# Performance work log

Hardware: AMD Instinct MI355X
Metric: run time of the kernel (lower is better)

## Reference

```python
import jax, jax.numpy as jnp
import numpy as np

B, T, D, H = 4, 2048, 1024, 16
HS = D // H  # head_size = 64
EPS = 1e-5


def _layernorm(x, g, b):
    mu = jnp.mean(x, axis=-1, keepdims=True)
    var = jnp.var(x, axis=-1, keepdims=True)
    return (x - mu) * jax.lax.rsqrt(var + EPS) * g + b


def setup_inputs() -> dict:
    key = jax.random.key(0)
    ks = jax.random.split(key, 12)
    s = lambda fan_in: 1.0 / np.sqrt(fan_in)
    return {
        "x": jax.random.normal(ks[0], (B, T, D), dtype=jnp.float32),
        # per-head projections, stacked: (H, D, HS)
        "Wq": jax.random.uniform(ks[1], (H, D, HS), jnp.float32, -s(D), s(D)),
        "Wk": jax.random.uniform(ks[2], (H, D, HS), jnp.float32, -s(D), s(D)),
        "Wv": jax.random.uniform(ks[3], (H, D, HS), jnp.float32, -s(D), s(D)),
        "Wo": jax.random.uniform(ks[4], (D, D), jnp.float32, -s(D), s(D)),
        "bo": jax.random.uniform(ks[5], (D,), jnp.float32, -s(D), s(D)),
        "W1": jax.random.uniform(ks[6], (D, 4 * D), jnp.float32, -s(D), s(D)),
        "b1": jax.random.uniform(ks[7], (4 * D,), jnp.float32, -s(D), s(D)),
        "W2": jax.random.uniform(ks[8], (4 * D, D), jnp.float32, -s(4 * D), s(4 * D)),
        "b2": jax.random.uniform(ks[9], (D,), jnp.float32, -s(4 * D), s(4 * D)),
        "g1": jnp.ones((D,), jnp.float32),
        "be1": jnp.zeros((D,), jnp.float32),
        "g2": jnp.ones((D,), jnp.float32),
        "be2": jnp.zeros((D,), jnp.float32),
    }


def reference(x, Wq, Wk, Wv, Wo, bo, W1, b1, W2, b2, g1, be1, g2, be2):
    # --- self-attention sublayer (pre-LN) ---
    h = _layernorm(x, g1, be1)                       # (B,T,D)
    q = jnp.einsum('btd,hds->bhts', h, Wq)           # (B,H,T,HS)
    k = jnp.einsum('btd,hds->bhts', h, Wk)
    v = jnp.einsum('btd,hds->bhts', h, Wv)
    scores = jnp.einsum('bhts,bhus->bhtu', q, k) * (HS ** -0.5)  # (B,H,T,T)
    causal = jnp.tril(jnp.ones((T, T), dtype=bool))
    scores = jnp.where(causal, scores, -jnp.inf)
    w = jax.nn.softmax(scores, axis=-1)
    attn = jnp.einsum('bhtu,bhus->bhts', w, v)       # (B,H,T,HS)
    attn = attn.transpose(0, 2, 1, 3).reshape(B, T, D)  # concat heads
    x = x + attn @ Wo + bo
    # --- feed-forward sublayer (pre-LN) ---
    h2 = _layernorm(x, g2, be2)
    x = x + jax.nn.relu(h2 @ W1 + b1) @ W2 + b2
    return x
```

## Files before the change

kernel.cpp:

```cpp
#include <hip/hip_runtime.h>
#include <hip/hip_bf16.h>
#include <cstddef>

#define B_ 4
#define T_ 2048
#define D_ 1024
#define H_ 16
#define HS_ 64
#define QS_ 3072

typedef short short8 __attribute__((ext_vector_type(8)));
typedef float f32x4 __attribute__((ext_vector_type(4)));

__device__ __forceinline__ unsigned short f2b(float x) {
    __hip_bfloat16 b = __float2bfloat16(x);
    return *reinterpret_cast<unsigned short*>(&b);
}

__device__ __forceinline__ void gload_lds16(const void* g, void* l) {
    __builtin_amdgcn_global_load_lds((const __attribute__((address_space(1))) void*)g,
                                     (__attribute__((address_space(3))) void*)l, 16, 0, 0);
}

__global__ __launch_bounds__(256) void ln_kernel(const float* __restrict__ X,
                                                 const float* __restrict__ g,
                                                 const float* __restrict__ be,
                                                 unsigned short* __restrict__ O)
{
    const int row = blockIdx.x;
    const int tid = threadIdx.x;
    const float* xr = X + (size_t)row * D_;
    float4 xv = *reinterpret_cast<const float4*>(xr + tid * 4);
    float s  = xv.x + xv.y + xv.z + xv.w;
    float s2 = xv.x * xv.x + xv.y * xv.y + xv.z * xv.z + xv.w * xv.w;
#pragma unroll
    for (int off = 32; off > 0; off >>= 1) {
        s  += __shfl_xor(s,  off);
        s2 += __shfl_xor(s2, off);
    }
    __shared__ float red[8];
    const int wid = tid >> 6, lane = tid & 63;
    if (lane == 0) { red[wid * 2] = s; red[wid * 2 + 1] = s2; }
    __syncthreads();
    s  = red[0] + red[2] + red[4] + red[6];
    s2 = red[1] + red[3] + red[5] + red[7];
    const float mu  = s * (1.0f / D_);
    const float var = s2 * (1.0f / D_) - mu * mu;
    const float r   = rsqrtf(var + 1e-5f);
    float4 gv = *reinterpret_cast<const float4*>(g  + tid * 4);
    float4 bv = *reinterpret_cast<const float4*>(be + tid * 4);
    ushort4 ov;
    ov.x = f2b((xv.x - mu) * r * gv.x + bv.x);
    ov.y = f2b((xv.y - mu) * r * gv.y + bv.y);
    ov.z = f2b((xv.z - mu) * r * gv.z + bv.z);
    ov.w = f2b((xv.w - mu) * r * gv.w + bv.w);
    *reinterpret_cast<ushort4*>(O + (size_t)row * D_ + tid * 4) = ov;
}

__global__ __launch_bounds__(256) void transpose_all(const float* __restrict__ Wq,
                                                     const float* __restrict__ Wk,
                                                     const float* __restrict__ Wv,
                                                     const float* __restrict__ Wo,
                                                     const float* __restrict__ W1,
                                                     const float* __restrict__ W2,
                                                     unsigned short* __restrict__ Wtqkv,
                                                     unsigned short* __restrict__ Wto,
                                                     unsigned short* __restrict__ Wt1,
                                                     unsigned short* __restrict__ Wt2)
{
    __shared__ float tile[32][33];
    const int tx = threadIdx.x & 31, ty = threadIdx.x >> 5;
    int s = blockIdx.x;

    if (s < 3072) {
        const float* in = (s < 1024) ? Wq : (s < 2048) ? Wk : Wv;
        const int noff = (s < 1024) ? 0 : (s < 2048) ? D_ : 2 * D_;
        s &= 1023;
        const int bn = (s & 31) * 32, bk = (s >> 5) * 32;
        const int head = bn >> 6, s0 = bn & 63;
#pragma unroll
        for (int i = 0; i < 32; i += 8)
            tile[ty + i][tx] = in[(size_t)head * D_ * HS_ + (size_t)(bk + ty + i) * HS_ + s0 + tx];
        __syncthreads();
#pragma unroll
        for (int i = 0; i < 32; i += 8)
            Wtqkv[(size_t)(noff + bn + ty + i) * D_ + bk + tx] = f2b(tile[tx][ty + i]);
        return;
    }
    s -= 3072;
    const float* in; unsigned short* out; int K, N, bn, bk;
    if (s < 1024)      { in = Wo; out = Wto; K = D_;     N = D_;     bn = (s & 31) * 32;  bk = (s >> 5) * 32; }
    else if (s < 5120) { s -= 1024; in = W1; out = Wt1; K = D_;     N = 4 * D_; bn = (s & 127) * 32; bk = (s >> 7) * 32; }
    else               { s -= 5120; in = W2; out = Wt2; K = 4 * D_; N = D_;     bn = (s & 31) * 32;  bk = (s >> 5) * 32; }
#pragma unroll
    for (int i = 0; i < 32; i += 8)
        tile[ty + i][tx] = in[(size_t)(bk + ty + i) * N + bn + tx];
    __syncthreads();
#pragma unroll
    for (int i = 0; i < 32; i += 8)
        out[(size_t)(bn + ty + i) * K + bk + tx] = f2b(tile[tx][ty + i]);
}

template<bool BIAS, bool RELU, bool RESID, bool OUT_BF16, bool SCALEQ>
__global__ __launch_bounds__(512, 1) void gemm_sq(const unsigned short* __restrict__ A,
                                                  const unsigned short* __restrict__ Bt,
                                                  const float* __restrict__ bias,
                                                  const float* __restrict__ resid,
                                                  float* __restrict__ Cf,
                                                  unsigned short* __restrict__ Cb,
                                                  int M, int N, int K)
{
    constexpr int BUFS = 16384 + 16384;
    __shared__ __attribute__((aligned(128))) unsigned short lds[2 * BUFS];

    const int tid = threadIdx.x, l = tid & 63, w = tid >> 6;
    const int wRow = w >> 2, wCol = w & 3;
    const int lr = l & 15, lq = l >> 4;

    const int gx = gridDim.x;
    const int nwg = gx * (int)gridDim.y;
    const int orig = (int)blockIdx.y * gx + (int)blockIdx.x;
    const int xcd = orig & 7, lo = orig >> 3;
    const int q8 = nwg >> 3, r8 = nwg & 7;
    const int wg = (xcd < r8 ? xcd * (q8 + 1) : r8 * (q8 + 1) + (xcd - r8) * q8) + lo;
    const int bm = wg / gx, bn = wg % gx;

    const int nt = K >> 6;

    auto ISSUE_HALF = [&](int t, int half) {
        const size_t kof = (size_t)t * 64;
        const int buf = t & 1;
        const unsigned short* src = (half < 2) ? A : Bt;
        const int rb = ((half < 2) ? bm : bn) * 256 + (half & 1) * 128;
        const int lb = buf * BUFS + ((half >= 2) ? 16384 : 0) + (half & 1) * 128 * 64;
#pragma unroll
        for (int p = 0; p < 2; ++p) {
            const int j = p * 512 + tid;
            const int row = j >> 3, ci = j & 7;
            gload_lds16(src + (size_t)(rb + row) * K + kof + ((ci ^ (row & 7)) * 8),
                        &lds[lb + j * 8]);
        }
    };

    f32x4 acc[8][4];
#pragma unroll
    for (int i = 0; i < 8; ++i)
#pragma unroll
        for (int j = 0; j < 4; ++j) acc[i][j] = (f32x4){0.f, 0.f, 0.f, 0.f};

    short8 af[4][2], bf[4][2];
    const int swz = lr & 7;

#pragma unroll
    for (int h = 0; h < 4; ++h) ISSUE_HALF(0, h);

    for (int t = 0; t < nt; ++t) {
        const unsigned short* As = &lds[(t & 1) * BUFS];
        const unsigned short* Bs = As + 16384;
        const bool more = (t + 1 < nt);

        asm volatile("s_waitcnt vmcnt(0)" ::: "memory");
        __builtin_amdgcn_s_barrier();

        if (more) ISSUE_HALF(t + 1, 0);
#pragma unroll
        for (int mi = 0; mi < 4; ++mi) {
            const int row = wRow * 128 + mi * 16 + lr;
#pragma unroll
            for (int ks = 0; ks < 2; ++ks)
                af[mi][ks] = *reinterpret_cast<const short8*>(&As[row * 64 + (((ks * 4 + lq) ^ swz) * 8)]);
        }
#pragma unroll
        for (int nj = 0; nj < 2; ++nj) {
            const int rowB = wCol * 64 + nj * 16 + lr;
#pragma unroll
            for (int ks = 0; ks < 2; ++ks)
                bf[nj][ks] = *reinterpret_cast<const short8*>(&Bs[rowB * 64 + (((ks * 4 + lq) ^ swz) * 8)]);
        }
        asm volatile("s_waitcnt lgkmcnt(0)" ::: "memory");
        __builtin_amdgcn_sched_barrier(0);
        __builtin_amdgcn_s_setprio(1);
#pragma unroll
        for (int mi = 0; mi < 4; ++mi)
#pragma unroll
            for (int nj = 0; nj < 2; ++nj)
#pragma unroll
                for (int ks = 0; ks < 2; ++ks)
                    acc[mi][nj] = __builtin_amdgcn_mfma_f32_16x16x32_bf16(af[mi][ks], bf[nj][ks], acc[mi][nj], 0, 0, 0);
        __builtin_amdgcn_s_setprio(0);

        if (more) ISSUE_HALF(t + 1, 1);
#pragma unroll
        for (int nj = 2; nj < 4; ++nj) {
            const int rowB = wCol * 64 + nj * 16 + lr;
#pragma unroll
            for (int ks = 0; ks < 2; ++ks)
                bf[nj][ks] = *reinterpret_cast<const short8*>(&Bs[rowB * 64 + (((ks * 4 + lq) ^ swz) * 8)]);
        }
        asm volatile("s_waitcnt lgkmcnt(0)" ::: "memory");
        __builtin_amdgcn_sched_barrier(0);
        __builtin_amdgcn_s_setprio(1);
#pragma unroll
        for (int mi = 0; mi < 4; ++mi)
#pragma unroll
            for (int nj = 2; nj < 4; ++nj)
#pragma unroll
                for (int ks = 0; ks < 2; ++ks)
                    acc[mi][nj] = __builtin_amdgcn_mfma_f32_16x16x32_bf16(af[mi][ks], bf[nj][ks], acc[mi][nj], 0, 0, 0);
        __builtin_amdgcn_s_setprio(0);

        if (more) { ISSUE_HALF(t + 1, 2); ISSUE_HALF(t + 1, 3); }
#pragma unroll
        for (int mi = 0; mi < 4; ++mi) {
            const int row = wRow * 128 + (4 + mi) * 16 + lr;
#pragma unroll
            for (int ks = 0; ks < 2; ++ks)
                af[mi][ks] = *reinterpret_cast<const short8*>(&As[row * 64 + (((ks * 4 + lq) ^ swz) * 8)]);
        }
        asm volatile("s_waitcnt lgkmcnt(0)" ::: "memory");
        __builtin_amdgcn_sched_barrier(0);
        __builtin_amdgcn_s_setprio(1);
#pragma unroll
        for (int mi = 0; mi < 4; ++mi)
#pragma unroll
            for (int nj = 0; nj < 2; ++nj)
#pragma unroll
                for (int ks = 0; ks < 2; ++ks)
                    acc[4 + mi][nj] = __builtin_amdgcn_mfma_f32_16x16x32_bf16(af[mi][ks], bf[nj][ks], acc[4 + mi][nj], 0, 0, 0);
        __builtin_amdgcn_s_setprio(0);

        __builtin_amdgcn_s_setprio(1);
#pragma unroll
        for (int mi = 0; mi < 4; ++mi)
#pragma unroll
            for (int nj = 2; nj < 4; ++nj)
#pragma unroll
                for (int ks = 0; ks < 2; ++ks)
                    acc[4 + mi][nj] = __builtin_amdgcn_mfma_f32_16x16x32_bf16(af[mi][ks], bf[nj][ks], acc[4 + mi][nj], 0, 0, 0);
        __builtin_amdgcn_s_setprio(0);
    }

    const int m0 = bm * 256 + wRow * 128;
    const int n0 = bn * 256 + wCol * 64;
#pragma unroll
    for (int nf = 0; nf < 4; ++nf) {
        const int col = n0 + nf * 16 + lr;
        const float bv = BIAS ? bias[col] : 0.0f;
#pragma unroll
        for (int mf = 0; mf < 8; ++mf) {
#pragma unroll
            for (int r = 0; r < 4; ++r) {
                const int row = m0 + mf * 16 + lq * 4 + r;
                float c = acc[mf][nf][r] + bv;
                if (RELU) c = fmaxf(c, 0.0f);
                if (RESID) c += resid[(size_t)row * N + col];
                if (SCALEQ) { if (col < D_) c *= 0.18033688f; }
                if (OUT_BF16) Cb[(size_t)row * N + col] = f2b(c);
                else          Cf[(size_t)row * N + col] = c;
            }
        }
    }
}

template<bool BIAS, bool RELU, bool RESID, bool OUT_BF16, bool SCALEQ, bool VSPLIT>
__global__ __launch_bounds__(512, 1) void gemm_sq2(const unsigned short* __restrict__ A,
                                                   const unsigned short* __restrict__ Bt,
                                                   const float* __restrict__ bias,
                                                   const float* __restrict__ resid,
                                                   float* __restrict__ Cf,
                                                   unsigned short* __restrict__ Cb,
                                                   unsigned short* __restrict__ Vt,
                                                   int M, int N, int K)
{
    constexpr int BUFS = 8192 + 16384;
    __shared__ __attribute__((aligned(128))) unsigned short lds[3 * BUFS];

    const int tid = threadIdx.x, l = tid & 63, w = tid >> 6;
    const int wRow = w >> 2, wCol = w & 3;
    const int lr = l & 15, lq = l >> 4;

    const int gx = gridDim.x;
    const int nwg = gx * (int)gridDim.y;
    const int orig = (int)blockIdx.y * gx + (int)blockIdx.x;
    const int xcd = orig & 7, lo = orig >> 3;
    const int q8 = nwg >> 3, r8 = nwg & 7;
    const int wg = (xcd < r8 ? xcd * (q8 + 1) : r8 * (q8 + 1) + (xcd - r8) * q8) + lo;
    const int bm = wg / gx, bn = wg % gx;

    const int nt = K >> 6;

    auto ISSUE = [&](int t, int buf) {
        const size_t kof = (size_t)t * 64;
#pragma unroll
        for (int p = 0; p < 2; ++p) {
            const int j = p * 512 + tid;
            const int row = j >> 3, ci = j & 7;
            gload_lds16(A + (size_t)(bm * 128 + row) * K + kof + ((ci ^ (row & 7)) * 8),
                        &lds[buf * BUFS + j * 8]);
        }
#pragma unroll
        for (int p = 0; p < 4; ++p) {
            const int j = p * 512 + tid;
            const int row = j >> 3, ci = j & 7;
            gload_lds16(Bt + (size_t)(bn * 256 + row) * K + kof + ((ci ^ (row & 7)) * 8),
                        &lds[buf * BUFS + 8192 + j * 8]);
        }
    };

    f32x4 acc[4][4];
#pragma unroll
    for (int i = 0; i < 4; ++i)
#pragma unroll
        for (int j = 0; j < 4; ++j) acc[i][j] = (f32x4){0.f, 0.f, 0.f, 0.f};

    short8 af[2][2], bf[4][2];
    const int swz = lr & 7;

    ISSUE(0, 0);
    ISSUE(1, 1);

    for (int t = 0; t < nt; ++t) {
        const unsigned short* As = &lds[(t % 3) * BUFS];
        const unsigned short* Bs = As + 8192;
        if (t + 1 < nt) asm volatile("s_waitcnt vmcnt(6)" ::: "memory");
        else            asm volatile("s_waitcnt vmcnt(0)" ::: "memory");
        __builtin_amdgcn_s_barrier();
        if (t + 2 < nt) ISSUE(t + 2, (t + 2) % 3);

#pragma unroll
        for (int mi = 0; mi < 2; ++mi) {
            const int row = wRow * 64 + mi * 16 + lr;
#pragma unroll
            for (int ks = 0; ks < 2; ++ks)
                af[mi][ks] = *reinterpret_cast<const short8*>(&As[row * 64 + (((ks * 4 + lq) ^ swz) * 8)]);
        }
#pragma unroll
        for (int nj = 0; nj < 4; ++nj) {
            const int rowB = wCol * 64 + nj * 16 + lr;
#pragma unroll
            for (int ks = 0; ks < 2; ++ks)
                bf[nj][ks] = *reinterpret_cast<const short8*>(&Bs[rowB * 64 + (((ks * 4 + lq) ^ swz) * 8)]);
        }
        asm volatile("s_waitcnt lgkmcnt(0)" ::: "memory");
        __builtin_amdgcn_sched_barrier(0);
        __builtin_amdgcn_s_setprio(1);
#pragma unroll
        for (int mi = 0; mi < 2; ++mi)
#pragma unroll
            for (int nj = 0; nj < 4; ++nj)
#pragma unroll
                for (int ks = 0; ks < 2; ++ks)
                    acc[mi][nj] = __builtin_amdgcn_mfma_f32_16x16x32_bf16(af[mi][ks], bf[nj][ks], acc[mi][nj], 0, 0, 0);
        __builtin_amdgcn_s_setprio(0);

#pragma unroll
        for (int mi = 0; mi < 2; ++mi) {
            const int row = wRow * 64 + (2 + mi) * 16 + lr;
#pragma unroll
            for (int ks = 0; ks < 2; ++ks)
                af[mi][ks] = *reinterpret_cast<const short8*>(&As[row * 64 + (((ks * 4 + lq) ^ swz) * 8)]);
        }
        asm volatile("s_waitcnt lgkmcnt(0)" ::: "memory");
        __builtin_amdgcn_sched_barrier(0);
        __builtin_amdgcn_s_setprio(1);
#pragma unroll
        for (int mi = 0; mi < 2; ++mi)
#pragma unroll
            for (int nj = 0; nj < 4; ++nj)
#pragma unroll
                for (int ks = 0; ks < 2; ++ks)
                    acc[2 + mi][nj] = __builtin_amdgcn_mfma_f32_16x16x32_bf16(af[mi][ks], bf[nj][ks], acc[2 + mi][nj], 0, 0, 0);
        __builtin_amdgcn_s_setprio(0);
    }

    if (VSPLIT && bn >= 8) {
        __syncthreads();
        unsigned short* ldsT = lds;
        const int n0l = wCol * 64;
        const int m0l = wRow * 64;
#pragma unroll
        for (int nf = 0; nf < 4; ++nf) {
            const int cl = n0l + nf * 16 + lr;
#pragma unroll
            for (int mf = 0; mf < 4; ++mf) {
#pragma unroll
                for (int r = 0; r < 4; ++r) {
                    const int rl = m0l + mf * 16 + lq * 4 + r;
                    const int pos = (rl & 64) + (((rl & 15) << 2) | ((rl >> 4) & 3));
                    ldsT[cl * 136 + pos] = f2b(acc[mf][nf][r]);
                }
            }
        }
        __syncthreads();
        const int rowT = tid >> 1, half = tid & 1;
        const int colV = bn * 256 + rowT - 2 * D_;
        const int hd = colV >> 6, sdim = colV & 63;
        const int bb = bm >> 4;
        const int tt0 = (bm & 15) * 128 + half * 64;
        unsigned short* dst = Vt + (((size_t)(bb * H_ + hd) * 64 + sdim) << 11) + tt0;
        const unsigned short* srcl = &ldsT[rowT * 136 + half * 64];
#pragma unroll
        for (int i = 0; i < 8; ++i)
            *reinterpret_cast<short8*>(dst + i * 8) =
                *reinterpret_cast<const short8*>(srcl + i * 8);
        return;
    }

    const int m0 = bm * 128 + wRow * 64;
    const int n0 = bn * 256 + wCol * 64;
#pragma unroll
    for (int nf = 0; nf < 4; ++nf) {
        const int col = n0 + nf * 16 + lr;
        const float bv = BIAS ? bias[col] : 0.0f;
#pragma unroll
        for (int mf = 0; mf < 4; ++mf) {
#pragma unroll
            for (int r = 0; r < 4; ++r) {
                const int row = m0 + mf * 16 + lq * 4 + r;
                float c = acc[mf][nf][r] + bv;
                if (RELU) c = fmaxf(c, 0.0f);
                if (RESID) c += resid[(size_t)row * N + col];
                if (SCALEQ) { if (col < D_) c *= 0.18033688f; }
                if (OUT_BF16) Cb[(size_t)row * N + col] = f2b(c);
                else          Cf[(size_t)row * N + col] = c;
            }
        }
    }
}

template<bool MASKED>
__device__ __forceinline__ void attn_chunk(
    const unsigned short* __restrict__ ksb,
    const unsigned short* __restrict__ vsb,
    unsigned short (* __restrict__ psw)[72],
    const short8* aq, f32x4* o,
    int lr, int lq, int wl)
{
    const short8 vone = {0x3F80, 0x3F80, 0x3F80, 0x3F80, 0x3F80, 0x3F80, 0x3F80, 0x3F80};
    f32x4 s[4];
#pragma unroll
    for (int kb = 0; kb < 4; ++kb) s[kb] = (f32x4){0.f, 0.f, 0.f, 0.f};
    __builtin_amdgcn_s_setprio(1);
#pragma unroll
    for (int kb = 0; kb < 4; ++kb) {
        if (MASKED && kb > wl) continue;
        const int row = kb * 16 + lr;
        const int sw = row & 7;
#pragma unroll
        for (int ks = 0; ks < 2; ++ks) {
            const int ch = (ks * 4 + lq) ^ sw;
            const short8 bk = *reinterpret_cast<const short8*>(&ksb[row * 64 + ch * 8]);
            s[kb] = __builtin_amdgcn_mfma_f32_16x16x32_bf16(aq[ks], bk, s[kb], 0, 0, 0);
        }
    }
    __builtin_amdgcn_s_setprio(0);

#pragma unroll
    for (int r = 0; r < 4; ++r) {
        const int qloc = wl * 16 + lq * 4 + r;
        float p[4];
#pragma unroll
        for (int kb = 0; kb < 4; ++kb) {
            const bool msk = MASKED && (kb * 16 + lr > qloc);
            p[kb] = msk ? 0.0f : exp2f(s[kb][r]);
        }
        const unsigned int w0 = (unsigned int)f2b(p[0]) | ((unsigned int)f2b(p[1]) << 16);
        const unsigned int w1 = (unsigned int)f2b(p[2]) | ((unsigned int)f2b(p[3]) << 16);
        uint2 pk; pk.x = w0; pk.y = w1;
        *reinterpret_cast<uint2*>(&psw[lq * 4 + r][lr * 4]) = pk;
    }
    asm volatile("s_waitcnt lgkmcnt(0)" ::: "memory");
    __builtin_amdgcn_s_setprio(1);
#pragma unroll
    for (int ks = 0; ks < 2; ++ks) {
        const short8 pa = *reinterpret_cast<const short8*>(&psw[lr][ks * 32 + lq * 8]);
#pragma unroll
        for (int df = 0; df < 4; ++df) {
            const int vrow = df * 16 + lr;
            const int vch = (ks * 4 + lq) ^ (vrow & 7);
            const short8 vb = *reinterpret_cast<const short8*>(&vsb[vrow * 64 + vch * 8]);
            o[df] = __builtin_amdgcn_mfma_f32_16x16x32_bf16(pa, vb, o[df], 0, 0, 0);
        }
        o[4] = __builtin_amdgcn_mfma_f32_16x16x32_bf16(pa, vone, o[4], 0, 0, 0);
    }
    __builtin_amdgcn_s_setprio(0);
}

__global__ __launch_bounds__(512, 4) void attn_mfma(const unsigned short* __restrict__ QKV,
                                                    const unsigned short* __restrict__ Vt,
                                                    unsigned short* __restrict__ Og)
{
    __shared__ __attribute__((aligned(128))) unsigned short Ks[2][64 * 64];
    __shared__ __attribute__((aligned(128))) unsigned short Vs[2][64 * 64];
    __shared__ __attribute__((aligned(16)))  unsigned short Ps[8][16][72];

    const int NQT = T_ / 128;
    const int px = blockIdx.x;
    const int qtA = px, qtB = NQT - 1 - px;
    const int h = blockIdx.y, b = blockIdx.z;
    const int tid = threadIdx.x, w = tid >> 6, l = tid & 63;
    const int wl = w & 3, qsub = w >> 2;
    const int lr = l & 15, lq = l >> 4;
    const size_t base = (size_t)b * T_ * QS_ + h * HS_;

    short8 aqA[2], aqB[2];
    {
        const int qrl = qsub * 64 + wl * 16 + lr;
        const unsigned short* pA = QKV + base + (size_t)(qtA * 128 + qrl) * QS_;
        const unsigned short* pB = QKV + base + (size_t)(qtB * 128 + qrl) * QS_;
        aqA[0] = *reinterpret_cast<const short8*>(pA + lq * 8);
        aqA[1] = *reinterpret_cast<const short8*>(pA + 32 + lq * 8);
        aqB[0] = *reinterpret_cast<const short8*>(pB + lq * 8);
        aqB[1] = *reinterpret_cast<const short8*>(pB + 32 + lq * 8);
    }

    const unsigned short* Kg = QKV + D_;
    const unsigned short* Vg = Vt + ((size_t)(b * H_ + h) * 64 << 11);

    auto stage = [&](int c, int bf) {
        const int kbase = c * 64;
        const int row = tid >> 3;
        const int cx = ((tid & 7) ^ (row & 7)) * 8;
        gload_lds16(Kg + base + (size_t)(kbase + row) * QS_ + cx, &Ks[bf][tid * 8]);
        gload_lds16(Vg + ((size_t)row << 11) + kbase + cx, &Vs[bf][tid * 8]);
    };

    stage(0, 0);
    __syncthreads();

    unsigned short (*psw)[72] = Ps[w];

    f32x4 oA[5], oB[5];
#pragma unroll
    for (int df = 0; df < 5; ++df) {
        oA[df] = (f32x4){0.f, 0.f, 0.f, 0.f};
        oB[df] = (f32x4){0.f, 0.f, 0.f, 0.f};
    }

    const int qminw = qsub * 64 + wl * 16;
    const int qmaxw = qminw + 15;

    const int nch = 2 * qtB + 2;
    int bf = 0;
    for (int c = 0; c < nch; ++c) {
        if (c + 1 < nch) stage(c + 1, bf ^ 1);
        const int relA = c * 64 - qtA * 128;
        const int relB = c * 64 - qtB * 128;
        if (relA <= qmaxw) {
            if (relA + 63 <= qminw)
                attn_chunk<false>(&Ks[bf][0], &Vs[bf][0], psw, aqA, oA, lr, lq, wl);
            else
                attn_chunk<true>(&Ks[bf][0], &Vs[bf][0], psw, aqA, oA, lr, lq, wl);
        }
        if (relB <= qmaxw) {
            if (relB + 63 <= qminw)
                attn_chunk<false>(&Ks[bf][0], &Vs[bf][0], psw, aqB, oB, lr, lq, wl);
            else
                attn_chunk<true>(&Ks[bf][0], &Vs[bf][0], psw, aqB, oB, lr, lq, wl);
        }
        if (c + 1 < nch) __syncthreads();
        bf ^= 1;
    }

    const size_t obase = (size_t)b * T_ * D_ + h * HS_;
#pragma unroll
    for (int r = 0; r < 4; ++r) {
        const float invA = 1.0f / oA[4][r];
        const float invB = 1.0f / oB[4][r];
        const int qrl = qsub * 64 + wl * 16 + lq * 4 + r;
        unsigned short* orowA = Og + obase + (size_t)(qtA * 128 + qrl) * D_;
        unsigned short* orowB = Og + obase + (size_t)(qtB * 128 + qrl) * D_;
#pragma unroll
        for (int df = 0; df < 4; ++df) {
            orowA[df * 16 + lr] = f2b(oA[df][r] * invA);
            orowB[df * 16 + lr] = f2b(oB[df][r] * invB);
        }
    }
}

extern "C" void kernel_launch(void* const* d_in, const int* in_sizes, int n_in,
                              void* d_out, int out_size, void* d_ws, size_t ws_size,
                              hipStream_t stream)
{
    const float* x   = (const float*)d_in[0];
    const float* Wq  = (const float*)d_in[1];
    const float* Wk  = (const float*)d_in[2];
    const float* Wv  = (const float*)d_in[3];
    const float* Wo  = (const float*)d_in[4];
    const float* bo  = (const float*)d_in[5];
    const float* W1  = (const float*)d_in[6];
    const float* b1  = (const float*)d_in[7];
    const float* W2  = (const float*)d_in[8];
    const float* b2  = (const float*)d_in[9];
    const float* g1  = (const float*)d_in[10];
    const float* be1 = (const float*)d_in[11];
    const float* g2  = (const float*)d_in[12];
    const float* be2 = (const float*)d_in[13];
    float* out = (float*)d_out;

    unsigned short* ws = (unsigned short*)d_ws;
    const size_t NT = (size_t)B_ * T_;
    unsigned short* hb    = ws;
    unsigned short* QKVb  = hb + NT * D_;
    unsigned short* Ab    = QKVb + NT * 3 * D_;
    unsigned short* f1    = QKVb;
    unsigned short* Wtqkv = Ab + NT * D_;
    unsigned short* Wto   = Wtqkv + (size_t)3 * D_ * D_;
    unsigned short* Wt1   = Wto + (size_t)D_ * D_;
    unsigned short* Wt2   = Wt1 + (size_t)4 * D_ * D_;
    unsigned short* Vtb   = Wt2 + (size_t)4 * D_ * D_;

    dim3 b256(256), b512(512);

    transpose_all<<<dim3(12288), b256, 0, stream>>>(Wq, Wk, Wv, Wo, W1, W2,
                                                    Wtqkv, Wto, Wt1, Wt2);

    ln_kernel<<<NT, b256, 0, stream>>>(x, g1, be1, hb);

    gemm_sq2<false, false, false, true, true, true><<<dim3(3 * D_ / 256, NT / 128), b512, 0, stream>>>(
        hb, Wtqkv, nullptr, nullptr, nullptr, QKVb, Vtb, (int)NT, 3 * D_, D_);

    attn_mfma<<<dim3(T_ / 256, H_, B_), b512, 0, stream>>>(QKVb, Vtb, Ab);

    gemm_sq2<true, false, true, false, false, false><<<dim3(D_ / 256, NT / 128), b512, 0, stream>>>(
        Ab, Wto, bo, x, out, nullptr, nullptr, (int)NT, D_, D_);

    ln_kernel<<<NT, b256, 0, stream>>>(out, g2, be2, hb);

    gemm_sq<true, true, false, true, false><<<dim3(4 * D_ / 256, NT / 256), b512, 0, stream>>>(
        hb, Wt1, b1, nullptr, nullptr, f1, (int)NT, 4 * D_, D_);

    gemm_sq2<true, false, true, false, false, false><<<dim3(D_ / 256, NT / 128), b512, 0, stream>>>(
        f1, Wt2, b2, out, out, nullptr, nullptr, (int)NT, D_, 4 * D_);
}
```

Measured before the change: 330.2 us.

## Use four-stage K=32 LDS pipeline in the FFN up-projection GEMM

Replaces the double-buffered K=64 tile loop of the 256x256 FFN1 GEMM with a four-buffer ring of K=32 tiles, keeping up to three tiles in flight and using partial vmcnt waits instead of draining all loads each iteration. The LDS swizzle is adapted to 32-element rows. This aims to hide global-memory latency better behind the MFMA work, at the cost of twice as many barriers per K and a smaller compute block between synchronisations.

```diff
diff --git a/kernel.cpp b/kernel.cpp
--- a/kernel.cpp
+++ b/kernel.cpp
@@ -101,8 +101,8 @@
         out[(size_t)(bn + ty + i) * K + bk + tx] = f2b(tile[tx][ty + i]);
 }
 
-template<bool BIAS, bool RELU, bool RESID, bool OUT_BF16, bool SCALEQ>
-__global__ __launch_bounds__(512, 1) void gemm_sq(const unsigned short* __restrict__ A,
+template<bool BIAS, bool RELU, bool RESID, bool OUT_BF16>
+__global__ __launch_bounds__(512, 1) void gemm_p8(const unsigned short* __restrict__ A,
                                                   const unsigned short* __restrict__ Bt,
                                                   const float* __restrict__ bias,
                                                   const float* __restrict__ resid,
@@ -110,8 +110,8 @@
                                                   unsigned short* __restrict__ Cb,
                                                   int M, int N, int K)
 {
-    constexpr int BUFS = 16384 + 16384;
-    __shared__ __attribute__((aligned(128))) unsigned short lds[2 * BUFS];
+    constexpr int BUFS = 8192 + 8192;
+    __shared__ __attribute__((aligned(128))) unsigned short lds[4 * BUFS];
 
     const int tid = threadIdx.x, l = tid & 63, w = tid >> 6;
     const int wRow = w >> 2, wCol = w & 3;
@@ -125,22 +125,30 @@
     const int wg = (xcd < r8 ? xcd * (q8 + 1) : r8 * (q8 + 1) + (xcd - r8) * q8) + lo;
     const int bm = wg / gx, bn = wg % gx;
 
-    const int nt = K >> 6;
-
-    auto ISSUE_HALF = [&](int t, int half) {
-        const size_t kof = (size_t)t * 64;
-        const int buf = t & 1;
-        const unsigned short* src = (half < 2) ? A : Bt;
-        const int rb = ((half < 2) ? bm : bn) * 256 + (half & 1) * 128;
-        const int lb = buf * BUFS + ((half >= 2) ? 16384 : 0) + (half & 1) * 128 * 64;
+    const int nt = K >> 5;
+
+    auto ISSUE_A = [&](int t) {
+        const int buf = t & 3;
+        const size_t kof = (size_t)t * 32;
 #pragma unroll
         for (int p = 0; p < 2; ++p) {
             const int j = p * 512 + tid;
-            const int row = j >> 3, ci = j & 7;
-            gload_lds16(src + (size_t)(rb + row) * K + kof + ((ci ^ (row & 7)) * 8),
-                        &lds[lb + j * 8]);
+            const int row = j >> 2, ci = j & 3;
+            gload_lds16(A + (size_t)(bm * 256 + row) * K + kof + ((ci ^ ((row >> 1) & 3)) * 8),
+                        &lds[buf * BUFS + j * 8]);
         }
     };
+    auto ISSUE_B = [&](int t) {
+        const int buf = t & 3;
+        const size_t kof = (size_t)t * 32;
+#pragma unroll
+        for (int p = 0; p < 2; ++p) {
+            const int j = p * 512 + tid;
+            const int row = j >> 2, ci = j & 3;
+            gload_lds16(Bt + (size_t)(bn * 256 + row) * K + kof + ((ci ^ ((row >> 1) & 3)) * 8),
+                        &lds[buf * BUFS + 8192 + j * 8]);
+        }
+    };
 
     f32x4 acc[8][4];
 #pragma unroll
@@ -148,34 +156,31 @@
 #pragma unroll
         for (int j = 0; j < 4; ++j) acc[i][j] = (f32x4){0.f, 0.f, 0.f, 0.f};
 
-    short8 af[4][2], bf[4][2];
-    const int swz = lr & 7;
-
-#pragma unroll
-    for (int h = 0; h < 4; ++h) ISSUE_HALF(0, h);
+    short8 af[4], bf[4];
+
+    ISSUE_A(0); ISSUE_B(0);
+    if (nt > 1) { ISSUE_A(1); ISSUE_B(1); }
+    if (nt > 2) { ISSUE_A(2); ISSUE_B(2); }
 
     for (int t = 0; t < nt; ++t) {
-        const unsigned short* As = &lds[(t & 1) * BUFS];
-        const unsigned short* Bs = As + 16384;
-        const bool more = (t + 1 < nt);
-
-        asm volatile("s_waitcnt vmcnt(0)" ::: "memory");
+        const int rem = nt - 1 - t;
+        if (rem >= 2)      asm volatile("s_waitcnt vmcnt(8)" ::: "memory");
+        else if (rem == 1) asm volatile("s_waitcnt vmcnt(4)" ::: "memory");
+        else               asm volatile("s_waitcnt vmcnt(0)" ::: "memory");
         __builtin_amdgcn_s_barrier();
-
-        if (more) ISSUE_HALF(t + 1, 0);
+        const unsigned short* As = &lds[(t & 3) * BUFS];
+        const unsigned short* Bs = As + 8192;
+
+        if (t + 3 < nt) ISSUE_A(t + 3);
 #pragma unroll
         for (int mi = 0; mi < 4; ++mi) {
             const int row = wRow * 128 + mi * 16 + lr;
-#pragma unroll
-            for (int ks = 0; ks < 2; ++ks)
-                af[mi][ks] = *reinterpret_cast<const short8*>(&As[row * 64 + (((ks * 4 + lq) ^ swz) * 8)]);
-        }
-#pragma unroll
-        for (int nj = 0; nj < 2; ++nj) {
+            af[mi] = *reinterpret_cast<const short8*>(&As[row * 32 + ((lq ^ ((row >> 1) & 3)) * 8)]);
+        }
+#pragma unroll
+        for (int nj = 0; nj < 4; ++nj) {
             const int rowB = wCol * 64 + nj * 16 + lr;
-#pragma unroll
-            for (int ks = 0; ks < 2; ++ks)
-                bf[nj][ks] = *reinterpret_cast<const short8*>(&Bs[rowB * 64 + (((ks * 4 + lq) ^ swz) * 8)]);
+            bf[nj] = *reinterpret_cast<const short8*>(&Bs[rowB * 32 + ((lq ^ ((rowB >> 1) & 3)) * 8)]);
         }
         asm volatile("s_waitcnt lgkmcnt(0)" ::: "memory");
         __builtin_amdgcn_sched_barrier(0);
@@ -183,19 +188,15 @@
 #pragma unroll
         for (int mi = 0; mi < 4; ++mi)
 #pragma unroll
-            for (int nj = 0; nj < 2; ++nj)
-#pragma unroll
-                for (int ks = 0; ks < 2; ++ks)
-                    acc[mi][nj] = __builtin_amdgcn_mfma_f32_16x16x32_bf16(af[mi][ks], bf[nj][ks], acc[mi][nj], 0, 0, 0);
+            for (int nj = 0; nj < 4; ++nj)
+                acc[mi][nj] = __builtin_amdgcn_mfma_f32_16x16x32_bf16(af[mi], bf[nj], acc[mi][nj], 0, 0, 0);
         __builtin_amdgcn_s_setprio(0);
 
-        if (more) ISSUE_HALF(t + 1, 1);
-#pragma unroll
-        for (int nj = 2; nj < 4; ++nj) {
-            const int rowB = wCol * 64 + nj * 16 + lr;
-#pragma unroll
-            for (int ks = 0; ks < 2; ++ks)
-                bf[nj][ks] = *reinterpret_cast<const short8*>(&Bs[rowB * 64 + (((ks * 4 + lq) ^ swz) * 8)]);
+        if (t + 3 < nt) ISSUE_B(t + 3);
+#pragma unroll
+        for (int mi = 0; mi < 4; ++mi) {
+            const int row = wRow * 128 + (4 + mi) * 16 + lr;
+            af[mi] = *reinterpret_cast<const short8*>(&As[row * 32 + ((lq ^ ((row >> 1) & 3)) * 8)]);
         }
         asm volatile("s_waitcnt lgkmcnt(0)" ::: "memory");
         __builtin_amdgcn_sched_barrier(0);
@@ -203,40 +204,8 @@
 #pragma unroll
         for (int mi = 0; mi < 4; ++mi)
 #pragma unroll
-            for (int nj = 2; nj < 4; ++nj)
-#pragma unroll
-                for (int ks = 0; ks < 2; ++ks)
-                    acc[mi][nj] = __builtin_amdgcn_mfma_f32_16x16x32_bf16(af[mi][ks], bf[nj][ks], acc[mi][nj], 0, 0, 0);
-        __builtin_amdgcn_s_setprio(0);
-
-        if (more) { ISSUE_HALF(t + 1, 2); ISSUE_HALF(t + 1, 3); }
-#pragma unroll
-        for (int mi = 0; mi < 4; ++mi) {
-            const int row = wRow * 128 + (4 + mi) * 16 + lr;
-#pragma unroll
-            for (int ks = 0; ks < 2; ++ks)
-                af[mi][ks] = *reinterpret_cast<const short8*>(&As[row * 64 + (((ks * 4 + lq) ^ swz) * 8)]);
-        }
-        asm volatile("s_waitcnt lgkmcnt(0)" ::: "memory");
-        __builtin_amdgcn_sched_barrier(0);
-        __builtin_amdgcn_s_setprio(1);
-#pragma unroll
-        for (int mi = 0; mi < 4; ++mi)
-#pragma unroll
-            for (int nj = 0; nj < 2; ++nj)
-#pragma unroll
-                for (int ks = 0; ks < 2; ++ks)
-                    acc[4 + mi][nj] = __builtin_amdgcn_mfma_f32_16x16x32_bf16(af[mi][ks], bf[nj][ks], acc[4 + mi][nj], 0, 0, 0);
-        __builtin_amdgcn_s_setprio(0);
-
-        __builtin_amdgcn_s_setprio(1);
-#pragma unroll
-        for (int mi = 0; mi < 4; ++mi)
-#pragma unroll
-            for (int nj = 2; nj < 4; ++nj)
-#pragma unroll
-                for (int ks = 0; ks < 2; ++ks)
-                    acc[4 + mi][nj] = __builtin_amdgcn_mfma_f32_16x16x32_bf16(af[mi][ks], bf[nj][ks], acc[4 + mi][nj], 0, 0, 0);
+            for (int nj = 0; nj < 4; ++nj)
+                acc[4 + mi][nj] = __builtin_amdgcn_mfma_f32_16x16x32_bf16(af[mi], bf[nj], acc[4 + mi][nj], 0, 0, 0);
         __builtin_amdgcn_s_setprio(0);
     }
 
@@ -254,7 +223,6 @@
                 float c = acc[mf][nf][r] + bv;
                 if (RELU) c = fmaxf(c, 0.0f);
                 if (RESID) c += resid[(size_t)row * N + col];
-                if (SCALEQ) { if (col < D_) c *= 0.18033688f; }
                 if (OUT_BF16) Cb[(size_t)row * N + col] = f2b(c);
                 else          Cf[(size_t)row * N + col] = c;
             }
@@ -627,7 +595,7 @@
 
     ln_kernel<<<NT, b256, 0, stream>>>(out, g2, be2, hb);
 
-    gemm_sq<true, true, false, true, false><<<dim3(4 * D_ / 256, NT / 256), b512, 0, stream>>>(
+    gemm_p8<true, true, false, true><<<dim3(4 * D_ / 256, NT / 256), b512, 0, stream>>>(
         hb, Wt1, b1, nullptr, nullptr, f1, (int)NT, 4 * D_, D_);
 
     gemm_sq2<true, false, true, false, false, false><<<dim3(D_ / 256, NT / 128), b512, 0, stream>>>(
```

New measurement: 337.6 us. +2.2%, slower.
